# Optimization experiments

Measured on AMD Instinct MI355X. Metric: run time of the kernel, lower is better.

Reference implementation:

```python
import jax, jax.numpy as jnp
import numpy as np

N = 4096
N_FEAT = 1024
N_HID = 8
N_HEADS = 8
N_CLASSES = 16
ALPHA = 0.2
NEG_BIG = -9e15


def setup_inputs() -> dict:
    key = jax.random.key(0)
    ks = jax.random.split(key, 6)
    x = jax.random.normal(ks[0], (N, N_FEAT), dtype=jnp.float32)
    adj = (jax.random.uniform(ks[1], (N, N)) < 0.01).astype(jnp.float32)
    adj = jnp.maximum(adj, jnp.eye(N, dtype=jnp.float32))
    W_heads = jax.random.normal(ks[2], (N_HEADS, N_FEAT, N_HID), dtype=jnp.float32) * 0.05
    a_heads = jax.random.normal(ks[3], (N_HEADS, 2 * N_HID, 1), dtype=jnp.float32) * 0.05
    W_final = jax.random.normal(ks[4], (N_HEADS * N_HID, N_CLASSES), dtype=jnp.float32) * 0.05
    a_final = jax.random.normal(ks[5], (2 * N_CLASSES, 1), dtype=jnp.float32) * 0.05
    return {"x": x, "adj": adj, "W_heads": W_heads, "a_heads": a_heads,
            "W_final": W_final, "a_final": a_final}


def gat_layer(h, adj, W, a):
    # h: [N, Fin], W: [Fin, Fout], a: [2*Fout, 1]
    Wh = h @ W                                  # [N, Fout]
    Fout = W.shape[1]
    f_src = Wh @ a[:Fout, 0]                    # [N] -- Wh_i . a[:F]
    f_dst = Wh @ a[Fout:, 0]                    # [N] -- Wh_j . a[F:]
    e = jax.nn.leaky_relu(f_src[:, None] + f_dst[None, :], ALPHA)  # [N, N]
    e = jnp.where(adj > 0, e, NEG_BIG)
    attention = jax.nn.softmax(e, axis=1)       # dropout skipped (eval mode)
    return attention @ Wh                        # [N, Fout]


def reference(x, adj, W_heads, a_heads, W_final, a_final):
    # multi-head GAT layer (8 independent heads), concat along features
    heads = jax.vmap(lambda W, a: gat_layer(x, adj, W, a))(W_heads, a_heads)  # [H, N, n_hid]
    h = jnp.transpose(heads, (1, 0, 2)).reshape(x.shape[0], -1)               # [N, H*n_hid]
    h = jax.nn.elu(h)
    out = gat_layer(h, adj, W_final, a_final)    # [N, n_classes]
    return jax.nn.log_softmax(out, axis=1)
```

## Files before the change

kernel.cpp:

```cpp
#include <hip/hip_runtime.h>
#include <math.h>

#define N 4096
#define NFEAT 1024
#define NHID 8
#define NHEADS 8
#define NCLS 16
#define CAP 128

#define GEMM_BLOCKS 512

__global__ __launch_bounds__(256) void ka_scan_gemm(const float* __restrict__ adj,
                                                    const float* __restrict__ x,
                                                    const float* __restrict__ W_heads,
                                                    const float* __restrict__ a_heads,
                                                    int* __restrict__ deg,
                                                    int* __restrict__ nbr,
                                                    float* __restrict__ Wh,
                                                    float* __restrict__ fsrc,
                                                    float* __restrict__ fdst) {
    __shared__ float smem[8 * NFEAT + 4 * 8 * 64];
    const int tid = threadIdx.x;

    if (blockIdx.x >= GEMM_BLOCKS) {
        const int sb = blockIdx.x - GEMM_BLOCKS;
        const int wave = tid >> 6, lane = tid & 63;
        const int row = sb * 4 + wave;
        const float4* arow = (const float4*)(adj + (size_t)row * N);
        int* outl = nbr + (size_t)row * CAP;

        float4 v[16];
        #pragma unroll
        for (int i = 0; i < 16; ++i) v[i] = arow[lane + i * 64];

        const unsigned long long below_mask = (1ull << lane) - 1ull;
        int base = 0;
        #pragma unroll
        for (int i = 0; i < 16; ++i) {
            #pragma unroll
            for (int e = 0; e < 4; ++e) {
                const float val = e == 0 ? v[i].x : e == 1 ? v[i].y
                                : e == 2 ? v[i].z : v[i].w;
                const bool pred = val > 0.f;
                const unsigned long long bal = __ballot(pred);
                const int p = base + __popcll(bal & below_mask);
                if (pred && p < CAP) outl[p] = (lane + i * 64) * 4 + e;
                base += __popcll(bal);
            }
        }
        if (lane == 0) deg[row] = base > CAP ? CAP : base;
        return;
    }

    float* xs = smem;
    float (*red)[8][64] = (float (*)[8][64])(smem + 8 * NFEAT);
    const int w = tid >> 6, c = tid & 63;
    const int row0 = blockIdx.x * 8;

    const float4* xg = (const float4*)(x + (size_t)row0 * NFEAT);
    float4* xls = (float4*)xs;
    #pragma unroll
    for (int i = 0; i < 8; ++i) xls[tid + i * 256] = xg[tid + i * 256];
    __syncthreads();

    float acc[8] = {};
    const float* wp = W_heads + (size_t)(c >> 3) * (NFEAT * NHID) + (c & 7)
                    + (size_t)(w * 256) * NHID;
    const float* xw = xs + w * 256;
    for (int k = 0; k < 256; k += 8) {
        float wv[8];
        #pragma unroll
        for (int u = 0; u < 8; ++u) wv[u] = wp[(k + u) * 8];
        #pragma unroll
        for (int r = 0; r < 8; ++r) {
            const float4 a0 = *(const float4*)(xw + r * NFEAT + k);
            const float4 a1 = *(const float4*)(xw + r * NFEAT + k + 4);
            acc[r] += a0.x * wv[0] + a0.y * wv[1] + a0.z * wv[2] + a0.w * wv[3]
                    + a1.x * wv[4] + a1.y * wv[5] + a1.z * wv[6] + a1.w * wv[7];
        }
    }
    #pragma unroll
    for (int r = 0; r < 8; ++r) red[w][r][c] = acc[r];
    __syncthreads();
    #pragma unroll
    for (int e0 = 0; e0 < 2; ++e0) {
        int e = tid + e0 * 256;
        int r = e >> 6, cc = e & 63;
        float v = red[0][r][cc] + red[1][r][cc] + red[2][r][cc] + red[3][r][cc];
        Wh[(size_t)(row0 + r) * 64 + cc] = v;
        int h = cc >> 3, kh = cc & 7;
        float vs = v * a_heads[h * 16 + kh];
        float vd = v * a_heads[h * 16 + 8 + kh];
        vs += __shfl_xor(vs, 1); vs += __shfl_xor(vs, 2); vs += __shfl_xor(vs, 4);
        vd += __shfl_xor(vd, 1); vd += __shfl_xor(vd, 2); vd += __shfl_xor(vd, 4);
        if (kh == 0) { fsrc[h * N + row0 + r] = vs; fdst[h * N + row0 + r] = vd; }
    }
}

__global__ __launch_bounds__(256) void kb_attn1(const float* __restrict__ fsrc,
                                                const float* __restrict__ fdst,
                                                const float* __restrict__ Wh,
                                                const int* __restrict__ deg,
                                                const int* __restrict__ nbr,
                                                const float* __restrict__ W_final,
                                                const float* __restrict__ a_final,
                                                float* __restrict__ Wh2,
                                                float* __restrict__ fsrc2,
                                                float* __restrict__ fdst2) {
    __shared__ float hrow[4][64];
    const int wave = threadIdx.x >> 6;
    const int lane = threadIdx.x & 63;
    const int row = blockIdx.x * 4 + wave;
    const int h = lane >> 3;
    const int nn = lane & 7;
    const int d = deg[row];
    const int* nl = nbr + (size_t)row * CAP;
    const float fs = fsrc[h * N + row];
    const float* fd = fdst + h * N;

    float pacc[8] = {0.f, 0.f, 0.f, 0.f, 0.f, 0.f, 0.f, 0.f};
    float sp = 0.f;

    #pragma unroll
    for (int r = 0; r < 16; ++r) {
        if (r * 8 < d) {
            const int n = r * 8 + nn;
            const bool vv = n < d;
            const int j = vv ? nl[n] : 0;
            const float e = fs + fd[j];
            const float w = vv ? __expf(fmaxf(e, 0.2f * e)) : 0.f;
            sp += w;
            const float4 wv0 = *(const float4*)(Wh + (size_t)j * 64 + h * 8);
            const float4 wv1 = *(const float4*)(Wh + (size_t)j * 64 + h * 8 + 4);
            pacc[0] += w * wv0.x; pacc[1] += w * wv0.y;
            pacc[2] += w * wv0.z; pacc[3] += w * wv0.w;
            pacc[4] += w * wv1.x; pacc[5] += w * wv1.y;
            pacc[6] += w * wv1.z; pacc[7] += w * wv1.w;
        }
    }

    sp += __shfl_xor(sp, 1);
    sp += __shfl_xor(sp, 2);
    sp += __shfl_xor(sp, 4);

    const int k0 = nn & 1, k1 = (nn >> 1) & 1, k2 = nn >> 2;
    float t0 = (k0 ? pacc[1] : pacc[0]) + __shfl_xor(k0 ? pacc[0] : pacc[1], 1);
    float t1 = (k0 ? pacc[3] : pacc[2]) + __shfl_xor(k0 ? pacc[2] : pacc[3], 1);
    float t2 = (k0 ? pacc[5] : pacc[4]) + __shfl_xor(k0 ? pacc[4] : pacc[5], 1);
    float t3 = (k0 ? pacc[7] : pacc[6]) + __shfl_xor(k0 ? pacc[6] : pacc[7], 1);
    float u0 = (k1 ? t1 : t0) + __shfl_xor(k1 ? t0 : t1, 2);
    float u1 = (k1 ? t3 : t2) + __shfl_xor(k1 ? t2 : t3, 2);
    float of = (k2 ? u1 : u0) + __shfl_xor(k2 ? u0 : u1, 4);

    float o = of / sp;
    o = o > 0.f ? o : (__expf(o) - 1.f);
    hrow[wave][lane] = o;
    __syncthreads();

    const int g = lane >> 4, cc = lane & 15;
    float p = 0.f;
    #pragma unroll
    for (int f0 = 0; f0 < 16; ++f0) {
        int f = g * 16 + f0;
        p += hrow[wave][f] * W_final[f * 16 + cc];
    }
    p += __shfl_xor(p, 16);
    p += __shfl_xor(p, 32);
    if (g == 0) Wh2[(size_t)row * 16 + cc] = p;
    float vs = p * a_final[cc];
    float vd = p * a_final[16 + cc];
    #pragma unroll
    for (int mm = 1; mm < 16; mm <<= 1) {
        vs += __shfl_xor(vs, mm);
        vd += __shfl_xor(vd, mm);
    }
    if (lane == 0) { fsrc2[row] = vs; fdst2[row] = vd; }
}

__global__ __launch_bounds__(256) void kc_attn2(const float* __restrict__ fsrc2,
                                                const float* __restrict__ fdst2,
                                                const float* __restrict__ Wh2,
                                                const int* __restrict__ deg,
                                                const int* __restrict__ nbr,
                                                float* __restrict__ out) {
    const int wave = threadIdx.x >> 6;
    const int lane = threadIdx.x & 63;
    const int row = blockIdx.x * 4 + wave;
    const int jj = lane >> 4, c = lane & 15;
    const int d = deg[row];
    const int* nl = nbr + (size_t)row * CAP;
    const float fs = fsrc2[row];

    const bool v0 = lane < d;
    const int jl0 = v0 ? nl[lane] : 0;
    const float e0 = fs + fdst2[jl0];
    const float w0 = v0 ? __expf(fmaxf(e0, 0.2f * e0)) : 0.f;

    int jl1 = 0;
    float w1 = 0.f;
    if (__builtin_expect(d > 64, 0)) {
        const bool v1 = 64 + lane < d;
        const int jx = v1 ? nl[64 + lane] : 0;
        jl1 = jx;
        const float e1 = fs + fdst2[jx];
        w1 = v1 ? __expf(fmaxf(e1, 0.2f * e1)) : 0.f;
    }

    float s = w0 + w1;
    #pragma unroll
    for (int mm = 1; mm < 64; mm <<= 1) s += __shfl_xor(s, mm);

    const int dc = d < 64 ? d : 64;
    float acc = 0.f, acc2 = 0.f;
    int n = jj;
    for (; n + 4 < dc; n += 8) {
        const int ja = __shfl(jl0, n);
        const float wa = __shfl(w0, n);
        const int jb = __shfl(jl0, n + 4);
        const float wb = __shfl(w0, n + 4);
        acc  += wa * Wh2[(size_t)ja * 16 + c];
        acc2 += wb * Wh2[(size_t)jb * 16 + c];
    }
    if (n < dc) {
        const int ja = __shfl(jl0, n);
        const float wa = __shfl(w0, n);
        acc += wa * Wh2[(size_t)ja * 16 + c];
    }
    if (__builtin_expect(d > 64, 0)) {
        for (int m = 64 + jj; m < d; m += 4) {
            const int jb = __shfl(jl1, m - 64);
            const float wb = __shfl(w1, m - 64);
            acc2 += wb * Wh2[(size_t)jb * 16 + c];
        }
    }
    acc += acc2;
    acc += __shfl_xor(acc, 16);
    acc += __shfl_xor(acc, 32);

    float u = acc / s;
    float m2 = u;
    #pragma unroll
    for (int mm = 1; mm < 16; mm <<= 1) m2 = fmaxf(m2, __shfl_xor(m2, mm));
    float tv = u - m2;
    float se = __expf(tv);
    #pragma unroll
    for (int mm = 1; mm < 16; mm <<= 1) se += __shfl_xor(se, mm);
    float o = tv - logf(se);
    if (jj == 0) out[(size_t)row * 16 + c] = o;
}

extern "C" void kernel_launch(void* const* d_in, const int* in_sizes, int n_in,
                              void* d_out, int out_size, void* d_ws, size_t ws_size,
                              hipStream_t stream) {
    const float* x       = (const float*)d_in[0];
    const float* adj     = (const float*)d_in[1];
    const float* W_heads = (const float*)d_in[2];
    const float* a_heads = (const float*)d_in[3];
    const float* W_final = (const float*)d_in[4];
    const float* a_final = (const float*)d_in[5];
    float* out = (float*)d_out;

    float* ws    = (float*)d_ws;
    float* Wh    = ws;
    float* fsrc  = Wh + 262144;
    float* fdst  = fsrc + 32768;
    float* Wh2   = fdst + 32768;
    float* fsrc2 = Wh2 + 65536;
    float* fdst2 = fsrc2 + 4096;
    int*   deg   = (int*)(fdst2 + 4096);
    int*   nbr   = deg + 4096;

    ka_scan_gemm<<<GEMM_BLOCKS + N / 4, 256, 0, stream>>>(adj, x, W_heads, a_heads,
                                                          deg, nbr, Wh, fsrc, fdst);
    kb_attn1    <<<N / 4, 256, 0, stream>>>(fsrc, fdst, Wh, deg, nbr,
                                            W_final, a_final, Wh2, fsrc2, fdst2);
    kc_attn2    <<<N / 4, 256, 0, stream>>>(fsrc2, fdst2, Wh2, deg, nbr, out);
}
```

Measured before the change: 135.3 us.

## Co-locate adjacency scan waves with GEMM waves in 512-thread blocks

Replaces the separate scan blocks with 512-thread blocks in which waves 0-3 do the per-row GEMM and waves 4-7 each scan two adjacency rows, in two half-row chunks. The memory-bound scan and the compute-bound GEMM now share each block, so they can overlap on the same CU and fewer blocks are launched. Scan waves hit __syncthreads to match the GEMM path's barriers. This risks deadlock if the barrier counts differ, and the aggressive launch bounds (512,8) may force register caps and spills.

```diff
diff --git a/kernel.cpp b/kernel.cpp
--- a/kernel.cpp
+++ b/kernel.cpp
@@ -8,35 +8,37 @@
 #define NCLS 16
 #define CAP 128
 
-#define GEMM_BLOCKS 512
-
-__global__ __launch_bounds__(256) void ka_scan_gemm(const float* __restrict__ adj,
-                                                    const float* __restrict__ x,
-                                                    const float* __restrict__ W_heads,
-                                                    const float* __restrict__ a_heads,
-                                                    int* __restrict__ deg,
-                                                    int* __restrict__ nbr,
-                                                    float* __restrict__ Wh,
-                                                    float* __restrict__ fsrc,
-                                                    float* __restrict__ fdst) {
+__global__ __launch_bounds__(512, 8) void ka_scan_gemm(const float* __restrict__ adj,
+                                                       const float* __restrict__ x,
+                                                       const float* __restrict__ W_heads,
+                                                       const float* __restrict__ a_heads,
+                                                       int* __restrict__ deg,
+                                                       int* __restrict__ nbr,
+                                                       float* __restrict__ Wh,
+                                                       float* __restrict__ fsrc,
+                                                       float* __restrict__ fdst) {
     __shared__ float smem[8 * NFEAT + 4 * 8 * 64];
     const int tid = threadIdx.x;
-
-    if (blockIdx.x >= GEMM_BLOCKS) {
-        const int sb = blockIdx.x - GEMM_BLOCKS;
-        const int wave = tid >> 6, lane = tid & 63;
-        const int row = sb * 4 + wave;
-        const float4* arow = (const float4*)(adj + (size_t)row * N);
-        int* outl = nbr + (size_t)row * CAP;
-
-        float4 v[16];
-        #pragma unroll
-        for (int i = 0; i < 16; ++i) v[i] = arow[lane + i * 64];
-
+    const int wave = tid >> 6;
+    const int lane = tid & 63;
+    const int row0 = blockIdx.x * 8;
+
+    if (wave >= 4) {
+        const int sw = wave - 4;
         const unsigned long long below_mask = (1ull << lane) - 1ull;
+
+        const int rowA = row0 + sw * 2;
+        const float4* arA = (const float4*)(adj + (size_t)rowA * N);
+        int* outA = nbr + (size_t)rowA * CAP;
+        float4 v[8];
+        #pragma unroll
+        for (int i = 0; i < 8; ++i) v[i] = arA[lane + i * 64];
+
+        __syncthreads();
+
         int base = 0;
         #pragma unroll
-        for (int i = 0; i < 16; ++i) {
+        for (int i = 0; i < 8; ++i) {
             #pragma unroll
             for (int e = 0; e < 4; ++e) {
                 const float val = e == 0 ? v[i].x : e == 1 ? v[i].y
@@ -44,18 +46,70 @@
                 const bool pred = val > 0.f;
                 const unsigned long long bal = __ballot(pred);
                 const int p = base + __popcll(bal & below_mask);
-                if (pred && p < CAP) outl[p] = (lane + i * 64) * 4 + e;
+                if (pred && p < CAP) outA[p] = (lane + i * 64) * 4 + e;
                 base += __popcll(bal);
             }
         }
-        if (lane == 0) deg[row] = base > CAP ? CAP : base;
+        #pragma unroll
+        for (int i = 0; i < 8; ++i) v[i] = arA[lane + (8 + i) * 64];
+        #pragma unroll
+        for (int i = 0; i < 8; ++i) {
+            #pragma unroll
+            for (int e = 0; e < 4; ++e) {
+                const float val = e == 0 ? v[i].x : e == 1 ? v[i].y
+                                : e == 2 ? v[i].z : v[i].w;
+                const bool pred = val > 0.f;
+                const unsigned long long bal = __ballot(pred);
+                const int p = base + __popcll(bal & below_mask);
+                if (pred && p < CAP) outA[p] = (lane + (8 + i) * 64) * 4 + e;
+                base += __popcll(bal);
+            }
+        }
+        if (lane == 0) deg[rowA] = base > CAP ? CAP : base;
+
+        const int rowB = rowA + 1;
+        const float4* arB = (const float4*)(adj + (size_t)rowB * N);
+        int* outB = nbr + (size_t)rowB * CAP;
+        base = 0;
+        #pragma unroll
+        for (int i = 0; i < 8; ++i) v[i] = arB[lane + i * 64];
+        #pragma unroll
+        for (int i = 0; i < 8; ++i) {
+            #pragma unroll
+            for (int e = 0; e < 4; ++e) {
+                const float val = e == 0 ? v[i].x : e == 1 ? v[i].y
+                                : e == 2 ? v[i].z : v[i].w;
+                const bool pred = val > 0.f;
+                const unsigned long long bal = __ballot(pred);
+                const int p = base + __popcll(bal & below_mask);
+                if (pred && p < CAP) outB[p] = (lane + i * 64) * 4 + e;
+                base += __popcll(bal);
+            }
+        }
+        #pragma unroll
+        for (int i = 0; i < 8; ++i) v[i] = arB[lane + (8 + i) * 64];
+        #pragma unroll
+        for (int i = 0; i < 8; ++i) {
+            #pragma unroll
+            for (int e = 0; e < 4; ++e) {
+                const float val = e == 0 ? v[i].x : e == 1 ? v[i].y
+                                : e == 2 ? v[i].z : v[i].w;
+                const bool pred = val > 0.f;
+                const unsigned long long bal = __ballot(pred);
+                const int p = base + __popcll(bal & below_mask);
+                if (pred && p < CAP) outB[p] = (lane + (8 + i) * 64) * 4 + e;
+                base += __popcll(bal);
+            }
+        }
+        if (lane == 0) deg[rowB] = base > CAP ? CAP : base;
+
+        __syncthreads();
         return;
     }
 
     float* xs = smem;
     float (*red)[8][64] = (float (*)[8][64])(smem + 8 * NFEAT);
-    const int w = tid >> 6, c = tid & 63;
-    const int row0 = blockIdx.x * 8;
+    const int w = wave, c = lane;
 
     const float4* xg = (const float4*)(x + (size_t)row0 * NFEAT);
     float4* xls = (float4*)xs;
@@ -270,8 +324,8 @@
     int*   deg   = (int*)(fdst2 + 4096);
     int*   nbr   = deg + 4096;
 
-    ka_scan_gemm<<<GEMM_BLOCKS + N / 4, 256, 0, stream>>>(adj, x, W_heads, a_heads,
-                                                          deg, nbr, Wh, fsrc, fdst);
+    ka_scan_gemm<<<512, 512, 0, stream>>>(adj, x, W_heads, a_heads,
+                                          deg, nbr, Wh, fsrc, fdst);
     kb_attn1    <<<N / 4, 256, 0, stream>>>(fsrc, fdst, Wh, deg, nbr,
                                             W_final, a_final, Wh2, fsrc2, fdst2);
     kc_attn2    <<<N / 4, 256, 0, stream>>>(fsrc2, fdst2, Wh2, deg, nbr, out);
```

Result: slower. 143.8 us (+6.3%).

## Split fused scan/GEMM kernel into separate launches and prefetch weights

Applied to the files above, without the earlier changes.

The combined adjacency-scan and feature-GEMM kernel is split into two kernels so the scan kernel no longer reserves the GEMM's large shared-memory allocation, and it can run at higher occupancy with launch bounds of 8 blocks. The scan now loads the adjacency row in two halves of 8 float4 to reduce register pressure. The GEMM loop software-prefetches the next weight slice into registers. The trade-off is an extra kernel launch and the loss of overlap between the scan and GEMM work.

```diff
diff --git a/kernel.cpp b/kernel.cpp
--- a/kernel.cpp
+++ b/kernel.cpp
@@ -8,50 +8,59 @@
 #define NCLS 16
 #define CAP 128
 
-#define GEMM_BLOCKS 512
-
-__global__ __launch_bounds__(256) void ka_scan_gemm(const float* __restrict__ adj,
-                                                    const float* __restrict__ x,
-                                                    const float* __restrict__ W_heads,
-                                                    const float* __restrict__ a_heads,
-                                                    int* __restrict__ deg,
-                                                    int* __restrict__ nbr,
-                                                    float* __restrict__ Wh,
-                                                    float* __restrict__ fsrc,
-                                                    float* __restrict__ fdst) {
+__global__ __launch_bounds__(256, 8) void kscan(const float* __restrict__ adj,
+                                                int* __restrict__ deg,
+                                                int* __restrict__ nbr) {
+    const int wave = threadIdx.x >> 6;
+    const int lane = threadIdx.x & 63;
+    const int row = blockIdx.x * 4 + wave;
+    const float4* arow = (const float4*)(adj + (size_t)row * N);
+    int* outl = nbr + (size_t)row * CAP;
+    const unsigned long long below_mask = (1ull << lane) - 1ull;
+
+    float4 v[8];
+    int base = 0;
+    #pragma unroll
+    for (int i = 0; i < 8; ++i) v[i] = arow[lane + i * 64];
+    #pragma unroll
+    for (int i = 0; i < 8; ++i) {
+        #pragma unroll
+        for (int e = 0; e < 4; ++e) {
+            const float val = e == 0 ? v[i].x : e == 1 ? v[i].y
+                            : e == 2 ? v[i].z : v[i].w;
+            const bool pred = val > 0.f;
+            const unsigned long long bal = __ballot(pred);
+            const int p = base + __popcll(bal & below_mask);
+            if (pred && p < CAP) outl[p] = (lane + i * 64) * 4 + e;
+            base += __popcll(bal);
+        }
+    }
+    #pragma unroll
+    for (int i = 0; i < 8; ++i) v[i] = arow[lane + (8 + i) * 64];
+    #pragma unroll
+    for (int i = 0; i < 8; ++i) {
+        #pragma unroll
+        for (int e = 0; e < 4; ++e) {
+            const float val = e == 0 ? v[i].x : e == 1 ? v[i].y
+                            : e == 2 ? v[i].z : v[i].w;
+            const bool pred = val > 0.f;
+            const unsigned long long bal = __ballot(pred);
+            const int p = base + __popcll(bal & below_mask);
+            if (pred && p < CAP) outl[p] = (lane + (8 + i) * 64) * 4 + e;
+            base += __popcll(bal);
+        }
+    }
+    if (lane == 0) deg[row] = base > CAP ? CAP : base;
+}
+
+__global__ __launch_bounds__(256) void kgemm(const float* __restrict__ x,
+                                             const float* __restrict__ W_heads,
+                                             const float* __restrict__ a_heads,
+                                             float* __restrict__ Wh,
+                                             float* __restrict__ fsrc,
+                                             float* __restrict__ fdst) {
     __shared__ float smem[8 * NFEAT + 4 * 8 * 64];
     const int tid = threadIdx.x;
-
-    if (blockIdx.x >= GEMM_BLOCKS) {
-        const int sb = blockIdx.x - GEMM_BLOCKS;
-        const int wave = tid >> 6, lane = tid & 63;
-        const int row = sb * 4 + wave;
-        const float4* arow = (const float4*)(adj + (size_t)row * N);
-        int* outl = nbr + (size_t)row * CAP;
-
-        float4 v[16];
-        #pragma unroll
-        for (int i = 0; i < 16; ++i) v[i] = arow[lane + i * 64];
-
-        const unsigned long long below_mask = (1ull << lane) - 1ull;
-        int base = 0;
-        #pragma unroll
-        for (int i = 0; i < 16; ++i) {
-            #pragma unroll
-            for (int e = 0; e < 4; ++e) {
-                const float val = e == 0 ? v[i].x : e == 1 ? v[i].y
-                                : e == 2 ? v[i].z : v[i].w;
-                const bool pred = val > 0.f;
-                const unsigned long long bal = __ballot(pred);
-                const int p = base + __popcll(bal & below_mask);
-                if (pred && p < CAP) outl[p] = (lane + i * 64) * 4 + e;
-                base += __popcll(bal);
-            }
-        }
-        if (lane == 0) deg[row] = base > CAP ? CAP : base;
-        return;
-    }
-
     float* xs = smem;
     float (*red)[8][64] = (float (*)[8][64])(smem + 8 * NFEAT);
     const int w = tid >> 6, c = tid & 63;
@@ -67,10 +76,15 @@
     const float* wp = W_heads + (size_t)(c >> 3) * (NFEAT * NHID) + (c & 7)
                     + (size_t)(w * 256) * NHID;
     const float* xw = xs + w * 256;
+
+    float wv[8];
+    #pragma unroll
+    for (int u = 0; u < 8; ++u) wv[u] = wp[u * 8];
     for (int k = 0; k < 256; k += 8) {
-        float wv[8];
-        #pragma unroll
-        for (int u = 0; u < 8; ++u) wv[u] = wp[(k + u) * 8];
+        float wn[8];
+        const int kn = (k + 8 < 256) ? k + 8 : k;
+        #pragma unroll
+        for (int u = 0; u < 8; ++u) wn[u] = wp[(kn + u) * 8];
         #pragma unroll
         for (int r = 0; r < 8; ++r) {
             const float4 a0 = *(const float4*)(xw + r * NFEAT + k);
@@ -78,6 +92,8 @@
             acc[r] += a0.x * wv[0] + a0.y * wv[1] + a0.z * wv[2] + a0.w * wv[3]
                     + a1.x * wv[4] + a1.y * wv[5] + a1.z * wv[6] + a1.w * wv[7];
         }
+        #pragma unroll
+        for (int u = 0; u < 8; ++u) wv[u] = wn[u];
     }
     #pragma unroll
     for (int r = 0; r < 8; ++r) red[w][r][c] = acc[r];
@@ -270,9 +286,9 @@
     int*   deg   = (int*)(fdst2 + 4096);
     int*   nbr   = deg + 4096;
 
-    ka_scan_gemm<<<GEMM_BLOCKS + N / 4, 256, 0, stream>>>(adj, x, W_heads, a_heads,
-                                                          deg, nbr, Wh, fsrc, fdst);
-    kb_attn1    <<<N / 4, 256, 0, stream>>>(fsrc, fdst, Wh, deg, nbr,
-                                            W_final, a_final, Wh2, fsrc2, fdst2);
-    kc_attn2    <<<N / 4, 256, 0, stream>>>(fsrc2, fdst2, Wh2, deg, nbr, out);
-}
+    kscan<<<N / 4, 256, 0, stream>>>(adj, deg, nbr);
+    kgemm<<<512, 256, 0, stream>>>(x, W_heads, a_heads, Wh, fsrc, fdst);
+    kb_attn1<<<N / 4, 256, 0, stream>>>(fsrc, fdst, Wh, deg, nbr,
+                                        W_final, a_final, Wh2, fsrc2, fdst2);
+    kc_attn2<<<N / 4, 256, 0, stream>>>(fsrc2, fdst2, Wh2, deg, nbr, out);
+}
```

After: 145.6 us. 7.6% more time.
